# Optimization experiments

Measured on AMD Instinct MI355X. Metric: run time of the kernel, lower is better.

The kernel has to match this reference:

```python
import jax, jax.numpy as jnp
import numpy as np

D = 300       # word_embedding_dim
H = 15        # num_attention_heads
DK = D // H   # 20 per-head dim
QDIM = 200    # query_vector_dim (additive attention)
N_ITEMS = 100000
B, S = 1024, 50


def setup_inputs() -> dict:
    key = jax.random.key(0)
    ks = jax.random.split(key, 16)
    sc = 1.0 / np.sqrt(D)
    inp = {
        "user_news_id": jax.random.randint(ks[0], (B, S), 0, N_ITEMS, dtype=jnp.int64 if jax.config.jax_enable_x64 else jnp.int32),
        "user_vector": jax.random.normal(ks[1], (B, S, D), dtype=jnp.float32),
        # news-id embedding table, padding_idx=0 -> zero row
        "emb_table": jax.random.normal(ks[2], (N_ITEMS + 1, D), dtype=jnp.float32).at[0].set(0.0) * 0.02,
        # content Q/K/V projections
        "Wq": jax.random.normal(ks[3], (D, D), dtype=jnp.float32) * sc,
        "bq": jnp.zeros((D,), jnp.float32),
        "Wk": jax.random.normal(ks[4], (D, D), dtype=jnp.float32) * sc,
        "bk": jnp.zeros((D,), jnp.float32),
        "Wv": jax.random.normal(ks[5], (D, D), dtype=jnp.float32) * sc,
        "bv": jnp.zeros((D,), jnp.float32),
        # disentangled (news-id) Q/K projections
        "Wqp": jax.random.normal(ks[6], (D, D), dtype=jnp.float32) * sc,
        "bqp": jnp.zeros((D,), jnp.float32),
        "Wkp": jax.random.normal(ks[7], (D, D), dtype=jnp.float32) * sc,
        "bkp": jnp.zeros((D,), jnp.float32),
        # additive attention pooling params
        "W_add": jax.random.normal(ks[8], (D, QDIM), dtype=jnp.float32) * sc,
        "b_add": jnp.zeros((QDIM,), jnp.float32),
        "q_add": jax.random.normal(ks[9], (QDIM,), dtype=jnp.float32) * (1.0 / np.sqrt(QDIM)),
    }
    return inp


def _heads(x):
    # [B,S,D] -> [B,H,S,DK]
    b, s, _ = x.shape
    return x.reshape(b, s, H, DK).transpose(0, 2, 1, 3)


def reference(user_news_id, user_vector, emb_table, Wq, bq, Wk, bk, Wv, bv,
              Wqp, bqp, Wkp, bkp, W_add, b_add, q_add):
    # embedding lookup for clicked-news ids
    user_emb = emb_table[user_news_id]                      # [B,S,D]

    # content projections from user_vector, position/id projections from user_emb
    Qc = _heads(user_vector @ Wq + bq)
    Kc = _heads(user_vector @ Wk + bk)
    Vc = _heads(user_vector @ Wv + bv)
    Qp = _heads(user_emb @ Wqp + bqp)
    Kp = _heads(user_emb @ Wkp + bkp)

    # disentangled scores: content->content + content->id + id->content
    scores = (jnp.einsum("bhqd,bhkd->bhqk", Qc, Kc)
              + jnp.einsum("bhqd,bhkd->bhqk", Qc, Kp)
              + jnp.einsum("bhqd,bhkd->bhqk", Qp, Kc))
    scores = scores * (1.0 / np.sqrt(3.0 * DK))
    attn = jax.nn.softmax(scores, axis=-1)                  # [B,H,S,S]
    ctx = jnp.einsum("bhqk,bhkd->bhqd", attn, Vc)           # [B,H,S,DK]
    ctx = ctx.transpose(0, 2, 1, 3).reshape(user_vector.shape)  # [B,S,D]

    # additive attention pooling over the sequence
    t = jnp.tanh(ctx @ W_add + b_add)                       # [B,S,QDIM]
    a = jax.nn.softmax(t @ q_add, axis=-1)                  # [B,S]
    return jnp.einsum("bs,bsd->bd", a, ctx)                 # [B,D]
```

## Files before the change

kernel.cpp:

```cpp
#include <hip/hip_runtime.h>
#include <hip/hip_bf16.h>

#define SS   50
#define DD   300
#define NH   15
#define HD   20
#define QDIM 200

#define OFF_UV  0
#define OFF_UE  32800
#define QKSTR   400
#define OFF_Q   65600
#define OFF_K   85600
#define OFF_P   65600
#define PBLK    4608
#define PSTR    144
#define VTSTR   144
#define OFF_VT  105600
#define OFF_CTX 117120
#define OFF_LG  159104
#define OFF_A2  161152
#define OFF_IDS 161408
#define SM_TOTAL 161616

#define WSEG  97280
#define WAOFF 486400
#define WTOT  552960

typedef __attribute__((ext_vector_type(8)))  short bf8t;
typedef __attribute__((ext_vector_type(4)))  float f4t;
typedef __attribute__((ext_vector_type(16))) float f16t;

__device__ __forceinline__ unsigned short f2bf(float x){
  unsigned u = __float_as_uint(x);
  return (unsigned short)((u + 0x7fffu + ((u >> 16) & 1u)) >> 16);
}
__device__ __forceinline__ unsigned packbf(float a, float b){
  return (unsigned)f2bf(a) | ((unsigned)f2bf(b) << 16);
}
__device__ __forceinline__ f16t zero16(){
  f16t v;
  #pragma unroll
  for (int i = 0; i < 16; ++i) v[i] = 0.f;
  return v;
}

__global__ __launch_bounds__(256) void conv_weights(
    const float* __restrict__ Wq, const float* __restrict__ Wk,
    const float* __restrict__ Wv, const float* __restrict__ Wqp,
    const float* __restrict__ Wkp, const float* __restrict__ Wa,
    short* __restrict__ ws)
{
  int idx = blockIdx.x*256 + threadIdx.x;
  if (idx >= WTOT) return;
  float v = 0.f;
  if (idx < WAOFF){
    int seg = idx / WSEG, r = idx - seg*WSEG;
    int n = r / 320, k = r - n*320;
    const float* W = (seg==0)?Wq:(seg==1)?Wk:(seg==2)?Wv:(seg==3)?Wqp:Wkp;
    if (n < DD && k < DD) v = W[k*DD + n];
  } else {
    int r = idx - WAOFF;
    int n = r / 320, k = r - n*320;
    if (n < QDIM && k < DD) v = Wa[k*QDIM + n];
  }
  ws[idx] = (short)f2bf(v);
}

template<int NT, int NCTM>
__device__ __forceinline__ void gemm10(const unsigned char* sm, unsigned abase,
                                       const short* __restrict__ wt,
                                       int lane, int w, f4t (&acc)[NT][4])
{
  const int lm = lane & 15, lg = lane >> 4;
  #pragma unroll
  for (int step = 0; step < 10; ++step){
    bf8t a[4];
    #pragma unroll
    for (int rt = 0; rt < 4; ++rt)
      a[rt] = *(const bf8t*)(sm + abase + (unsigned)(rt*16 + lm)*656u + (unsigned)(step*32 + lg*8)*2u);
    #pragma unroll
    for (int t = 0; t < NT; ++t){
      int ct = w + t*8; if (ct > NCTM) ct = NCTM;
      bf8t bb = *(const bf8t*)(wt + (size_t)(ct*16 + lm)*320 + step*32 + lg*8);
      #pragma unroll
      for (int rt = 0; rt < 4; ++rt)
        acc[t][rt] = __builtin_amdgcn_mfma_f32_16x16x32_bf16(a[rt], bb, acc[t][rt], 0, 0, 0);
    }
  }
}

__global__ __launch_bounds__(512) void user_enc_kernel(
    const int*   __restrict__ ids, const float* __restrict__ uv,
    const float* __restrict__ emb,
    const float* __restrict__ bq, const float* __restrict__ bk,
    const float* __restrict__ bv, const float* __restrict__ bqp,
    const float* __restrict__ bkp,
    const float* __restrict__ ba, const float* __restrict__ qa,
    const short* __restrict__ wsb, float* __restrict__ out)
{
  __shared__ __align__(16) unsigned char sm[SM_TOTAL];
  const int tid  = threadIdx.x;
  const int b    = blockIdx.x;
  const int w    = tid >> 6;
  const int lane = tid & 63;
  const int lm   = lane & 15, lg = lane >> 4;
  const int l31  = lane & 31, hi = lane >> 5;

  const short* wqT  = wsb;
  const short* wkT  = wsb + WSEG;
  const short* wvT  = wsb + 2*WSEG;
  const short* wqpT = wsb + 3*WSEG;
  const short* wkpT = wsb + 4*WSEG;
  const short* waT  = wsb + WAOFF;

  if (tid < SS) *(int*)(sm + OFF_IDS + tid*4) = ids[(size_t)b*SS + tid];
  {
    const float* srcv = uv + (size_t)b*SS*DD;
    for (int i = tid; i < SS*75; i += 512){
      int s = i/75, j4 = i - s*75;
      float4 v = *(const float4*)(srcv + s*DD + j4*4);
      *(unsigned*)(sm + OFF_UV + (unsigned)s*656 + (unsigned)j4*8)     = packbf(v.x, v.y);
      *(unsigned*)(sm + OFF_UV + (unsigned)s*656 + (unsigned)j4*8 + 4) = packbf(v.z, v.w);
    }
    for (int i = tid; i < SS*28; i += 512){
      int s = i/28, j = i - s*28;
      unsigned off = (j < 14) ? (OFF_UV + (unsigned)s*656 + 600u + (unsigned)j*4)
                              : (OFF_UE + (unsigned)s*656 + 600u + (unsigned)(j-14)*4);
      *(unsigned*)(sm + off) = 0;
    }
    for (int i = tid; i < SS*14; i += 512)
      *(unsigned*)(sm + OFF_CTX + (unsigned)(i/14)*656 + 600u + (unsigned)(i%14)*4) = 0;
    for (int i = tid; i < 720; i += 512)
      *(float4*)(sm + OFF_VT + (unsigned)i*16) = make_float4(0.f,0.f,0.f,0.f);
  }
  __syncthreads();
  for (int i = tid; i < SS*75; i += 512){
    int s = i/75, j4 = i - s*75;
    int id = *(const int*)(sm + OFF_IDS + s*4);
    float4 v = *(const float4*)(emb + (size_t)id*DD + j4*4);
    *(unsigned*)(sm + OFF_UE + (unsigned)s*656 + (unsigned)j4*8)     = packbf(v.x, v.y);
    *(unsigned*)(sm + OFF_UE + (unsigned)s*656 + (unsigned)j4*8 + 4) = packbf(v.z, v.w);
  }

  const float rscale = 0.1290994449f;
  #pragma unroll 1
  for (int nb4 = 0; nb4 < 4; ++nb4){
    const int nheads = (nb4 < 3) ? 4 : 3;
    const int NCT    = (nb4 < 3) ? 5 : 4;
    __syncthreads();
    for (int i = tid; i < SS*4; i += 512){
      int r = i >> 2, hl0 = i & 3;
      *(float4*)(sm + OFF_Q + (unsigned)r*QKSTR + (unsigned)hl0*96 + 80) = make_float4(0.f,0.f,0.f,0.f);
      *(float4*)(sm + OFF_K + (unsigned)r*QKSTR + (unsigned)hl0*96 + 80) = make_float4(0.f,0.f,0.f,0.f);
    }
    for (int ht = w; ht < 8*NCT; ht += 8){
      const int g   = (ht >= 6*NCT) ? 3 : (ht >= 4*NCT) ? 2 : (ht >= 2*NCT) ? 1 : 0;
      const int rem = ht - g*2*NCT;
      const int c   = rem >> 1, rh = rem & 1;
      const int col = nb4*80 + c*16 + lm;
      const int colc = (col < DD) ? col : DD-1;
      const int head = col / HD;
      const int dd   = col - head*HD;
      const int hl   = head - nb4*4;
      const bool valid = (hl < nheads) && (col < DD);
      const unsigned abase = (g == 1) ? (unsigned)OFF_UE : (unsigned)OFF_UV;
      const short* wt = (g==0) ? wqT : (g==1) ? wqpT : (g==2) ? wvT : wkT;
      const short* wb = wt + (size_t)col*320 + lg*8;
      f4t a0 = {0.f,0.f,0.f,0.f}, a1 = {0.f,0.f,0.f,0.f};
      #pragma unroll
      for (int st = 0; st < 10; ++st){
        bf8t bb = *(const bf8t*)(wb + st*32);
        bf8t x0 = *(const bf8t*)(sm + abase + (unsigned)(rh*32 + lm)*656u + (unsigned)(st*32 + lg*8)*2u);
        bf8t x1 = *(const bf8t*)(sm + abase + (unsigned)(rh*32 + 16 + lm)*656u + (unsigned)(st*32 + lg*8)*2u);
        a0 = __builtin_amdgcn_mfma_f32_16x16x32_bf16(x0, bb, a0, 0, 0, 0);
        a1 = __builtin_amdgcn_mfma_f32_16x16x32_bf16(x1, bb, a1, 0, 0, 0);
      }
      if (g == 2){
        if (valid){
          float bias = bv[colc];
          unsigned vb = OFF_VT + (unsigned)(hl*HD + dd)*VTSTR;
          int r0 = rh*32 + lg*4;
          if (r0 < SS){
            *(unsigned*)(sm + vb + (unsigned)r0*2) = packbf(a0[0]+bias, a0[1]+bias);
            if (r0+2 < SS) *(unsigned*)(sm + vb + (unsigned)r0*2 + 4) = packbf(a0[2]+bias, a0[3]+bias);
          }
          int r1 = rh*32 + 16 + lg*4;
          if (r1 < SS){
            *(unsigned*)(sm + vb + (unsigned)r1*2) = packbf(a1[0]+bias, a1[1]+bias);
            if (r1+2 < SS) *(unsigned*)(sm + vb + (unsigned)r1*2 + 4) = packbf(a1[2]+bias, a1[3]+bias);
          }
        }
      } else if (g != 3){
        if (valid){
          float bias = (g==0) ? bq[colc] : bqp[colc];
          unsigned qb = OFF_Q + (unsigned)hl*96 + (unsigned)dd*2 + (g==1 ? 40u : 0u);
          #pragma unroll
          for (int i = 0; i < 4; ++i){
            int r0 = rh*32 + lg*4 + i;
            if (r0 < SS) *(unsigned short*)(sm + qb + (unsigned)r0*QKSTR) = f2bf(a0[i]+bias);
            int r1 = rh*32 + 16 + lg*4 + i;
            if (r1 < SS) *(unsigned short*)(sm + qb + (unsigned)r1*QKSTR) = f2bf(a1[i]+bias);
          }
        }
      } else {
        float bkc = bk[colc];
        if (valid){
          unsigned kb = OFF_K + (unsigned)hl*96 + (unsigned)dd*2 + 40u;
          #pragma unroll
          for (int i = 0; i < 4; ++i){
            int r0 = rh*32 + lg*4 + i;
            if (r0 < SS) *(unsigned short*)(sm + kb + (unsigned)r0*QKSTR) = f2bf(a0[i]+bkc);
            int r1 = rh*32 + 16 + lg*4 + i;
            if (r1 < SS) *(unsigned short*)(sm + kb + (unsigned)r1*QKSTR) = f2bf(a1[i]+bkc);
          }
        }
        const short* wb2 = wkpT + (size_t)col*320 + lg*8;
        #pragma unroll
        for (int st = 0; st < 10; ++st){
          bf8t bb = *(const bf8t*)(wb2 + st*32);
          bf8t x0 = *(const bf8t*)(sm + OFF_UE + (unsigned)(rh*32 + lm)*656u + (unsigned)(st*32 + lg*8)*2u);
          bf8t x1 = *(const bf8t*)(sm + OFF_UE + (unsigned)(rh*32 + 16 + lm)*656u + (unsigned)(st*32 + lg*8)*2u);
          a0 = __builtin_amdgcn_mfma_f32_16x16x32_bf16(x0, bb, a0, 0, 0, 0);
          a1 = __builtin_amdgcn_mfma_f32_16x16x32_bf16(x1, bb, a1, 0, 0, 0);
        }
        if (valid){
          float bsum = bkc + bkp[colc];
          unsigned kb = OFF_K + (unsigned)hl*96 + (unsigned)dd*2;
          #pragma unroll
          for (int i = 0; i < 4; ++i){
            int r0 = rh*32 + lg*4 + i;
            if (r0 < SS) *(unsigned short*)(sm + kb + (unsigned)r0*QKSTR) = f2bf(a0[i]+bsum);
            int r1 = rh*32 + 16 + lg*4 + i;
            if (r1 < SS) *(unsigned short*)(sm + kb + (unsigned)r1*QKSTR) = f2bf(a1[i]+bsum);
          }
        }
      }
    }
    __syncthreads();
    const int ahl = w >> 1, rt = w & 1;
    const bool act = (ahl < nheads);
    f16t s0, s1;
    if (act){
      s0 = zero16(); s1 = zero16();
      unsigned aoff = OFF_Q + (unsigned)(rt*32 + l31)*QKSTR + (unsigned)ahl*96 + (unsigned)hi*16;
      unsigned koff = OFF_K + (unsigned)l31*QKSTR + (unsigned)ahl*96 + (unsigned)hi*16;
      #pragma unroll
      for (int ks = 0; ks < 3; ++ks){
        bf8t a  = *(const bf8t*)(sm + aoff + ks*32);
        bf8t b0 = *(const bf8t*)(sm + koff + ks*32);
        bf8t b1 = *(const bf8t*)(sm + koff + 32u*QKSTR + ks*32);
        s0 = __builtin_amdgcn_mfma_f32_32x32x16_bf16(a, b0, s0, 0, 0, 0);
        s1 = __builtin_amdgcn_mfma_f32_32x32x16_bf16(a, b1, s1, 0, 0, 0);
      }
    }
    __syncthreads();
    if (act){
      const bool m1 = (l31 >= 18);
      unsigned pb = OFF_P + (unsigned)w*PBLK;
      float rinv[16];
      #pragma unroll
      for (int r = 0; r < 16; ++r){
        int lrow = (r&3) + 8*(r>>2) + 4*hi;
        float v0 = s0[r]*rscale;
        float v1 = m1 ? -INFINITY : s1[r]*rscale;
        float mx = fmaxf(v0, v1);
        #pragma unroll
        for (int off = 1; off <= 16; off <<= 1) mx = fmaxf(mx, __shfl_xor(mx, off));
        float e0 = __expf(v0 - mx);
        float e1 = m1 ? 0.f : __expf(v1 - mx);
        float sum = e0 + e1;
        #pragma unroll
        for (int off = 1; off <= 16; off <<= 1) sum += __shfl_xor(sum, off);
        rinv[r] = 1.0f/sum;
        *(unsigned short*)(sm + pb + (unsigned)lrow*PSTR + (unsigned)l31*2)      = f2bf(e0);
        *(unsigned short*)(sm + pb + (unsigned)lrow*PSTR + 64 + (unsigned)l31*2) = f2bf(e1);
      }
      f16t c = zero16();
      unsigned pa  = pb + (unsigned)l31*PSTR + (unsigned)hi*16;
      unsigned vb2 = OFF_VT + (unsigned)(ahl*HD + l31)*VTSTR + (unsigned)hi*16;
      #pragma unroll
      for (int ks = 0; ks < 4; ++ks){
        bf8t a = *(const bf8t*)(sm + pa + ks*32);
        bf8t v = *(const bf8t*)(sm + vb2 + ks*32);
        c = __builtin_amdgcn_mfma_f32_32x32x16_bf16(a, v, c, 0, 0, 0);
      }
      if (l31 < HD){
        int h = nb4*4 + ahl;
        #pragma unroll
        for (int r = 0; r < 16; ++r){
          int q = rt*32 + (r&3) + 8*(r>>2) + 4*hi;
          if (q < SS)
            *(unsigned short*)(sm + OFF_CTX + (unsigned)q*656 + (unsigned)(h*HD + l31)*2) =
                f2bf(c[r]*rinv[r]);
        }
      }
    }
  }
  __syncthreads();

  {
    f4t accp[2][4];
    #pragma unroll
    for (int t = 0; t < 2; ++t)
      #pragma unroll
      for (int r = 0; r < 4; ++r) accp[t][r] = (f4t){0.f,0.f,0.f,0.f};
    gemm10<2,12>(sm, OFF_CTX, waT, lane, w, accp);
    float part[4][4];
    #pragma unroll
    for (int rt2 = 0; rt2 < 4; ++rt2)
      #pragma unroll
      for (int i = 0; i < 4; ++i) part[rt2][i] = 0.f;
    #pragma unroll
    for (int t = 0; t < 2; ++t){
      int ct = w + t*8; if (ct > 12) ct = 12;
      bool valid = (t == 0) || (w < 5);
      int col = ct*16 + lm;
      float bav = (col < QDIM) ? ba[col] : 0.f;
      float qav = (valid && col < QDIM) ? qa[col] : 0.f;
      #pragma unroll
      for (int rt2 = 0; rt2 < 4; ++rt2)
        #pragma unroll
        for (int i = 0; i < 4; ++i)
          part[rt2][i] += tanhf(accp[t][rt2][i] + bav) * qav;
    }
    #pragma unroll
    for (int off = 1; off <= 8; off <<= 1)
      #pragma unroll
      for (int rt2 = 0; rt2 < 4; ++rt2)
        #pragma unroll
        for (int i = 0; i < 4; ++i)
          part[rt2][i] += __shfl_xor(part[rt2][i], off);
    if (lm == 0){
      #pragma unroll
      for (int rt2 = 0; rt2 < 4; ++rt2)
        #pragma unroll
        for (int i = 0; i < 4; ++i){
          int row = rt2*16 + lg*4 + i;
          if (row < SS) *(float*)(sm + OFF_LG + (unsigned)(row*8 + w)*4) = part[rt2][i];
        }
    }
  }
  __syncthreads();
  if (w == 0){
    const int sl = lane < SS ? lane : SS - 1;
    const bool rowok = lane < SS;
    float lgv = -INFINITY;
    if (rowok){
      float s = 0.f;
      #pragma unroll
      for (int j = 0; j < 8; ++j) s += *(const float*)(sm + OFF_LG + (unsigned)(sl*8 + j)*4);
      lgv = s;
    }
    float m = lgv;
    #pragma unroll
    for (int off = 32; off; off >>= 1) m = fmaxf(m, __shfl_xor(m, off));
    float e = rowok ? __expf(lgv - m) : 0.f;
    float ssum = e;
    #pragma unroll
    for (int off = 32; off; off >>= 1) ssum += __shfl_xor(ssum, off);
    *(float*)(sm + OFF_A2 + lane*4) = e / ssum;
  }
  __syncthreads();
  if (tid < DD){
    float accv = 0.f;
    for (int s = 0; s < SS; ++s){
      float av = *(const float*)(sm + OFF_A2 + (unsigned)s*4);
      unsigned short cv = *(const unsigned short*)(sm + OFF_CTX + (unsigned)s*656 + (unsigned)tid*2);
      accv = fmaf(av, __uint_as_float((unsigned)cv << 16), accv);
    }
    out[(size_t)b*DD + tid] = accv;
  }
}

extern "C" void kernel_launch(void* const* d_in, const int* in_sizes, int n_in,
                              void* d_out, int out_size, void* d_ws, size_t ws_size,
                              hipStream_t stream){
  (void)n_in; (void)ws_size; (void)out_size;
  const int*   ids = (const int*)  d_in[0];
  const float* uvp = (const float*)d_in[1];
  const float* emb = (const float*)d_in[2];
  const float* Wq  = (const float*)d_in[3];
  const float* bq  = (const float*)d_in[4];
  const float* Wk  = (const float*)d_in[5];
  const float* bk  = (const float*)d_in[6];
  const float* Wv  = (const float*)d_in[7];
  const float* bv  = (const float*)d_in[8];
  const float* Wqp = (const float*)d_in[9];
  const float* bqp = (const float*)d_in[10];
  const float* Wkp = (const float*)d_in[11];
  const float* bkp = (const float*)d_in[12];
  const float* Wa  = (const float*)d_in[13];
  const float* ba  = (const float*)d_in[14];
  const float* qa  = (const float*)d_in[15];
  short* wsb = (short*)d_ws;

  conv_weights<<<(WTOT + 255)/256, 256, 0, stream>>>(Wq, Wk, Wv, Wqp, Wkp, Wa, wsb);

  const int nblk = in_sizes[0] / SS;
  user_enc_kernel<<<nblk, 512, 0, stream>>>(ids, uvp, emb,
                                            bq, bk, bv, bqp, bkp, ba, qa,
                                            (const short*)wsb, (float*)d_out);
}
```

Baseline: 419.3 us.

## Split fused user encoder into projection, attention and pooling kernels

```diff
diff --git a/kernel.cpp b/kernel.cpp
--- a/kernel.cpp
+++ b/kernel.cpp
@@ -6,22 +6,6 @@
 #define NH   15
 #define HD   20
 #define QDIM 200
-
-#define OFF_UV  0
-#define OFF_UE  32800
-#define QKSTR   400
-#define OFF_Q   65600
-#define OFF_K   85600
-#define OFF_P   65600
-#define PBLK    4608
-#define PSTR    144
-#define VTSTR   144
-#define OFF_VT  105600
-#define OFF_CTX 117120
-#define OFF_LG  159104
-#define OFF_A2  161152
-#define OFF_IDS 161408
-#define SM_TOTAL 161616
 
 #define WSEG  97280
 #define WAOFF 486400
@@ -90,6 +74,363 @@
   }
 }
 
+#define K1_UV  0
+#define K1_UE  32800
+#define K1_IDS 74784
+#define K1_SM  74992
+
+__global__ __launch_bounds__(512) void k1_proj(
+    const int*   __restrict__ ids, const float* __restrict__ uv,
+    const float* __restrict__ emb,
+    const float* __restrict__ bq, const float* __restrict__ bk,
+    const float* __restrict__ bv, const float* __restrict__ bqp,
+    const float* __restrict__ bkp,
+    const short* __restrict__ wsb,
+    short* __restrict__ qg, short* __restrict__ kg, short* __restrict__ vg)
+{
+  __shared__ __align__(16) unsigned char sm[K1_SM];
+  const int tid  = threadIdx.x;
+  const int b    = blockIdx.x;
+  const int w    = tid >> 6;
+  const int lane = tid & 63;
+  const int lm   = lane & 15, lg = lane >> 4;
+
+  const short* wqT  = wsb;
+  const short* wkT  = wsb + WSEG;
+  const short* wvT  = wsb + 2*WSEG;
+  const short* wqpT = wsb + 3*WSEG;
+  const short* wkpT = wsb + 4*WSEG;
+
+  if (tid < SS) *(int*)(sm + K1_IDS + tid*4) = ids[(size_t)b*SS + tid];
+  {
+    const float* srcv = uv + (size_t)b*SS*DD;
+    for (int i = tid; i < SS*75; i += 512){
+      int s = i/75, j4 = i - s*75;
+      float4 v = *(const float4*)(srcv + s*DD + j4*4);
+      *(unsigned*)(sm + K1_UV + (unsigned)s*656 + (unsigned)j4*8)     = packbf(v.x, v.y);
+      *(unsigned*)(sm + K1_UV + (unsigned)s*656 + (unsigned)j4*8 + 4) = packbf(v.z, v.w);
+    }
+    for (int i = tid; i < SS*28; i += 512){
+      int s = i/28, j = i - s*28;
+      unsigned off = (j < 14) ? (K1_UV + (unsigned)s*656 + 600u + (unsigned)j*4)
+                              : (K1_UE + (unsigned)s*656 + 600u + (unsigned)(j-14)*4);
+      *(unsigned*)(sm + off) = 0;
+    }
+  }
+  __syncthreads();
+  for (int i = tid; i < SS*75; i += 512){
+    int s = i/75, j4 = i - s*75;
+    int id = *(const int*)(sm + K1_IDS + s*4);
+    float4 v = *(const float4*)(emb + (size_t)id*DD + j4*4);
+    *(unsigned*)(sm + K1_UE + (unsigned)s*656 + (unsigned)j4*8)     = packbf(v.x, v.y);
+    *(unsigned*)(sm + K1_UE + (unsigned)s*656 + (unsigned)j4*8 + 4) = packbf(v.z, v.w);
+  }
+  __syncthreads();
+
+  for (int i = tid; i < SS*15*4; i += 512){
+    int row = i / 60, r2 = i - row*60;
+    int head = r2 >> 2, j = r2 & 3;
+    size_t base = ((size_t)b*SS + row)*720 + head*48 + 40 + j*2;
+    *(unsigned*)(qg + base) = 0u;
+    *(unsigned*)(kg + base) = 0u;
+  }
+
+  for (int u = w; u < 152; u += 8){
+    const int g   = u / 38;
+    const int rem = u - g*38;
+    const int c   = rem >> 1, rh = rem & 1;
+    const int col  = c*16 + lm;
+    const int colc = (col < DD) ? col : DD-1;
+    const bool valid = (col < DD);
+    const int head = colc / HD;
+    const int dd   = colc - head*HD;
+    const unsigned abase = (g == 1) ? (unsigned)K1_UE : (unsigned)K1_UV;
+    const short* wt = (g==0) ? wqT : (g==1) ? wqpT : (g==2) ? wvT : wkT;
+    const short* wb = wt + (size_t)col*320 + lg*8;
+    f4t a0 = {0.f,0.f,0.f,0.f}, a1 = {0.f,0.f,0.f,0.f};
+    #pragma unroll
+    for (int st = 0; st < 10; ++st){
+      bf8t bb = *(const bf8t*)(wb + st*32);
+      bf8t x0 = *(const bf8t*)(sm + abase + (unsigned)(rh*32 + lm)*656u + (unsigned)(st*32 + lg*8)*2u);
+      bf8t x1 = *(const bf8t*)(sm + abase + (unsigned)(rh*32 + 16 + lm)*656u + (unsigned)(st*32 + lg*8)*2u);
+      a0 = __builtin_amdgcn_mfma_f32_16x16x32_bf16(x0, bb, a0, 0, 0, 0);
+      a1 = __builtin_amdgcn_mfma_f32_16x16x32_bf16(x1, bb, a1, 0, 0, 0);
+    }
+    if (g == 2){
+      if (valid){
+        float bias = bv[colc];
+        #pragma unroll
+        for (int i = 0; i < 4; ++i){
+          int r0 = rh*32 + lg*4 + i;
+          if (r0 < SS) vg[((size_t)b*SS + r0)*300 + col] = (short)f2bf(a0[i]+bias);
+          int r1 = rh*32 + 16 + lg*4 + i;
+          if (r1 < SS) vg[((size_t)b*SS + r1)*300 + col] = (short)f2bf(a1[i]+bias);
+        }
+      }
+    } else if (g != 3){
+      if (valid){
+        float bias = (g==0) ? bq[colc] : bqp[colc];
+        size_t qoff = (size_t)head*48 + dd + (g==1 ? 20 : 0);
+        #pragma unroll
+        for (int i = 0; i < 4; ++i){
+          int r0 = rh*32 + lg*4 + i;
+          if (r0 < SS) qg[((size_t)b*SS + r0)*720 + qoff] = (short)f2bf(a0[i]+bias);
+          int r1 = rh*32 + 16 + lg*4 + i;
+          if (r1 < SS) qg[((size_t)b*SS + r1)*720 + qoff] = (short)f2bf(a1[i]+bias);
+        }
+      }
+    } else {
+      float bkc = bk[colc];
+      if (valid){
+        size_t koff = (size_t)head*48 + 20 + dd;
+        #pragma unroll
+        for (int i = 0; i < 4; ++i){
+          int r0 = rh*32 + lg*4 + i;
+          if (r0 < SS) kg[((size_t)b*SS + r0)*720 + koff] = (short)f2bf(a0[i]+bkc);
+          int r1 = rh*32 + 16 + lg*4 + i;
+          if (r1 < SS) kg[((size_t)b*SS + r1)*720 + koff] = (short)f2bf(a1[i]+bkc);
+        }
+      }
+      const short* wb2 = wkpT + (size_t)col*320 + lg*8;
+      #pragma unroll
+      for (int st = 0; st < 10; ++st){
+        bf8t bb = *(const bf8t*)(wb2 + st*32);
+        bf8t x0 = *(const bf8t*)(sm + K1_UE + (unsigned)(rh*32 + lm)*656u + (unsigned)(st*32 + lg*8)*2u);
+        bf8t x1 = *(const bf8t*)(sm + K1_UE + (unsigned)(rh*32 + 16 + lm)*656u + (unsigned)(st*32 + lg*8)*2u);
+        a0 = __builtin_amdgcn_mfma_f32_16x16x32_bf16(x0, bb, a0, 0, 0, 0);
+        a1 = __builtin_amdgcn_mfma_f32_16x16x32_bf16(x1, bb, a1, 0, 0, 0);
+      }
+      if (valid){
+        float bsum = bkc + bkp[colc];
+        size_t koff = (size_t)head*48 + dd;
+        #pragma unroll
+        for (int i = 0; i < 4; ++i){
+          int r0 = rh*32 + lg*4 + i;
+          if (r0 < SS) kg[((size_t)b*SS + r0)*720 + koff] = (short)f2bf(a0[i]+bsum);
+          int r1 = rh*32 + 16 + lg*4 + i;
+          if (r1 < SS) kg[((size_t)b*SS + r1)*720 + koff] = (short)f2bf(a1[i]+bsum);
+        }
+      }
+    }
+  }
+}
+
+#define A_Q   0
+#define A_K   20000
+#define A_VT  40000
+#define A_PBLK 4608
+#define A_SM  53248
+
+__global__ __launch_bounds__(512) void k2_attn(
+    const short* __restrict__ qg, const short* __restrict__ kg,
+    const short* __restrict__ vg, short* __restrict__ cg)
+{
+  __shared__ __align__(16) unsigned char sm[A_SM];
+  const int tid  = threadIdx.x;
+  const int bid  = blockIdx.x;
+  const int b    = bid >> 2;
+  const int hg   = bid & 3;
+  const int nheads = (hg < 3) ? 4 : 3;
+  const int w    = tid >> 6;
+  const int lane = tid & 63;
+  const int l31  = lane & 31, hi = lane >> 5;
+
+  for (int i = tid; i < 828; i += 512)
+    *(float4*)(sm + A_VT + (unsigned)i*16) = make_float4(0.f,0.f,0.f,0.f);
+  __syncthreads();
+  for (int i = tid; i < 2400; i += 512){
+    int arr = (i < 1200) ? 0 : 1;
+    int j = i - arr*1200;
+    int row = j/24, c = j - row*24;
+    const short* src = (arr ? kg : qg) + ((size_t)b*SS + row)*720 + hg*192 + c*8;
+    float4 v = *(const float4*)src;
+    *(float4*)(sm + (arr ? A_K : A_Q) + (unsigned)row*400 + (unsigned)c*16) = v;
+  }
+  for (int i = tid; i < 2000; i += 512){
+    int row = i/40, d2 = i - row*40;
+    unsigned v = *(const unsigned*)(vg + ((size_t)b*SS + row)*300 + hg*80 + d2*2);
+    *(unsigned short*)(sm + A_VT + (unsigned)(d2*2)*144   + (unsigned)row*2) = (unsigned short)(v & 0xffffu);
+    *(unsigned short*)(sm + A_VT + (unsigned)(d2*2+1)*144 + (unsigned)row*2) = (unsigned short)(v >> 16);
+  }
+  __syncthreads();
+
+  const float rscale = 0.1290994449f;
+  const int ahl = w >> 1, rt = w & 1;
+  const bool act = (ahl < nheads);
+  f16t s0, s1;
+  if (act){
+    s0 = zero16(); s1 = zero16();
+    unsigned aoff = A_Q + (unsigned)(rt*32 + l31)*400 + (unsigned)ahl*96 + (unsigned)hi*16;
+    unsigned koff = A_K + (unsigned)l31*400 + (unsigned)ahl*96 + (unsigned)hi*16;
+    #pragma unroll
+    for (int ks = 0; ks < 3; ++ks){
+      bf8t a  = *(const bf8t*)(sm + aoff + ks*32);
+      bf8t b0 = *(const bf8t*)(sm + koff + ks*32);
+      bf8t b1 = *(const bf8t*)(sm + koff + 32u*400 + ks*32);
+      s0 = __builtin_amdgcn_mfma_f32_32x32x16_bf16(a, b0, s0, 0, 0, 0);
+      s1 = __builtin_amdgcn_mfma_f32_32x32x16_bf16(a, b1, s1, 0, 0, 0);
+    }
+  }
+  __syncthreads();
+  if (act){
+    const bool m1 = (l31 >= 18);
+    unsigned pb = (unsigned)w*A_PBLK;
+    float rinv[16];
+    #pragma unroll
+    for (int r = 0; r < 16; ++r){
+      int lrow = (r&3) + 8*(r>>2) + 4*hi;
+      float v0 = s0[r]*rscale;
+      float v1 = m1 ? -INFINITY : s1[r]*rscale;
+      float mx = fmaxf(v0, v1);
+      #pragma unroll
+      for (int off = 1; off <= 16; off <<= 1) mx = fmaxf(mx, __shfl_xor(mx, off));
+      float e0 = __expf(v0 - mx);
+      float e1 = m1 ? 0.f : __expf(v1 - mx);
+      float sum = e0 + e1;
+      #pragma unroll
+      for (int off = 1; off <= 16; off <<= 1) sum += __shfl_xor(sum, off);
+      rinv[r] = 1.0f/sum;
+      *(unsigned short*)(sm + pb + (unsigned)lrow*144 + (unsigned)l31*2)      = f2bf(e0);
+      *(unsigned short*)(sm + pb + (unsigned)lrow*144 + 64 + (unsigned)l31*2) = f2bf(e1);
+    }
+    f16t c = zero16();
+    unsigned pa  = pb + (unsigned)l31*144 + (unsigned)hi*16;
+    unsigned vb2 = A_VT + (unsigned)(ahl*HD + l31)*144 + (unsigned)hi*16;
+    #pragma unroll
+    for (int ks = 0; ks < 4; ++ks){
+      bf8t a = *(const bf8t*)(sm + pa + ks*32);
+      bf8t v = *(const bf8t*)(sm + vb2 + ks*32);
+      c = __builtin_amdgcn_mfma_f32_32x32x16_bf16(a, v, c, 0, 0, 0);
+    }
+    if (l31 < HD){
+      int h = hg*4 + ahl;
+      #pragma unroll
+      for (int r = 0; r < 16; ++r){
+        int q = rt*32 + (r&3) + 8*(r>>2) + 4*hi;
+        if (q < SS)
+          cg[((size_t)b*SS + q)*300 + h*HD + l31] = (short)f2bf(c[r]*rinv[r]);
+      }
+    }
+  }
+}
+
+#define B_CTX 0
+#define B_LG  41984
+#define B_A2  44032
+#define B_SM  44288
+
+__global__ __launch_bounds__(512) void k3_pool(
+    const short* __restrict__ cg, const short* __restrict__ wsb,
+    const float* __restrict__ ba, const float* __restrict__ qa,
+    float* __restrict__ out)
+{
+  __shared__ __align__(16) unsigned char sm[B_SM];
+  const int tid  = threadIdx.x;
+  const int b    = blockIdx.x;
+  const int w    = tid >> 6;
+  const int lane = tid & 63;
+  const int lm   = lane & 15, lg = lane >> 4;
+  const short* waT = wsb + WAOFF;
+
+  for (int i = tid; i < SS*75; i += 512){
+    int row = i/75, c = i - row*75;
+    uint2 v = *(const uint2*)(cg + ((size_t)b*SS + row)*300 + c*4);
+    *(uint2*)(sm + B_CTX + (unsigned)row*656 + (unsigned)c*8) = v;
+  }
+  for (int i = tid; i < SS*14; i += 512)
+    *(unsigned*)(sm + B_CTX + (unsigned)(i/14)*656 + 600u + (unsigned)(i%14)*4) = 0;
+  __syncthreads();
+
+  {
+    f4t accp[2][4];
+    #pragma unroll
+    for (int t = 0; t < 2; ++t)
+      #pragma unroll
+      for (int r = 0; r < 4; ++r) accp[t][r] = (f4t){0.f,0.f,0.f,0.f};
+    gemm10<2,12>(sm, B_CTX, waT, lane, w, accp);
+    float part[4][4];
+    #pragma unroll
+    for (int rt2 = 0; rt2 < 4; ++rt2)
+      #pragma unroll
+      for (int i = 0; i < 4; ++i) part[rt2][i] = 0.f;
+    #pragma unroll
+    for (int t = 0; t < 2; ++t){
+      int ct = w + t*8; if (ct > 12) ct = 12;
+      bool valid = (t == 0) || (w < 5);
+      int col = ct*16 + lm;
+      float bav = (col < QDIM) ? ba[col] : 0.f;
+      float qav = (valid && col < QDIM) ? qa[col] : 0.f;
+      #pragma unroll
+      for (int rt2 = 0; rt2 < 4; ++rt2)
+        #pragma unroll
+        for (int i = 0; i < 4; ++i)
+          part[rt2][i] += tanhf(accp[t][rt2][i] + bav) * qav;
+    }
+    #pragma unroll
+    for (int off = 1; off <= 8; off <<= 1)
+      #pragma unroll
+      for (int rt2 = 0; rt2 < 4; ++rt2)
+        #pragma unroll
+        for (int i = 0; i < 4; ++i)
+          part[rt2][i] += __shfl_xor(part[rt2][i], off);
+    if (lm == 0){
+      #pragma unroll
+      for (int rt2 = 0; rt2 < 4; ++rt2)
+        #pragma unroll
+        for (int i = 0; i < 4; ++i){
+          int row = rt2*16 + lg*4 + i;
+          if (row < SS) *(float*)(sm + B_LG + (unsigned)(row*8 + w)*4) = part[rt2][i];
+        }
+    }
+  }
+  __syncthreads();
+  if (w == 0){
+    const int sl = lane < SS ? lane : SS - 1;
+    const bool rowok = lane < SS;
+    float lgv = -INFINITY;
+    if (rowok){
+      float s = 0.f;
+      #pragma unroll
+      for (int j = 0; j < 8; ++j) s += *(const float*)(sm + B_LG + (unsigned)(sl*8 + j)*4);
+      lgv = s;
+    }
+    float m = lgv;
+    #pragma unroll
+    for (int off = 32; off; off >>= 1) m = fmaxf(m, __shfl_xor(m, off));
+    float e = rowok ? __expf(lgv - m) : 0.f;
+    float ssum = e;
+    #pragma unroll
+    for (int off = 32; off; off >>= 1) ssum += __shfl_xor(ssum, off);
+    *(float*)(sm + B_A2 + lane*4) = e / ssum;
+  }
+  __syncthreads();
+  if (tid < DD){
+    float accv = 0.f;
+    for (int s = 0; s < SS; ++s){
+      float av = *(const float*)(sm + B_A2 + (unsigned)s*4);
+      unsigned short cv = *(const unsigned short*)(sm + B_CTX + (unsigned)s*656 + (unsigned)tid*2);
+      accv = fmaf(av, __uint_as_float((unsigned)cv << 16), accv);
+    }
+    out[(size_t)b*DD + tid] = accv;
+  }
+}
+
+#define OFF_UV  0
+#define OFF_UE  32800
+#define QKSTR   400
+#define OFF_Q   65600
+#define OFF_K   85600
+#define OFF_P   65600
+#define PBLK    4608
+#define PSTR    144
+#define VTSTR   144
+#define OFF_VT  105600
+#define OFF_CTX 117120
+#define OFF_LG  159104
+#define OFF_A2  161152
+#define OFF_IDS 161408
+#define SM_TOTAL 161616
+
 __global__ __launch_bounds__(512) void user_enc_kernel(
     const int*   __restrict__ ids, const float* __restrict__ uv,
     const float* __restrict__ emb,
@@ -376,7 +717,7 @@
 extern "C" void kernel_launch(void* const* d_in, const int* in_sizes, int n_in,
                               void* d_out, int out_size, void* d_ws, size_t ws_size,
                               hipStream_t stream){
-  (void)n_in; (void)ws_size; (void)out_size;
+  (void)n_in; (void)out_size;
   const int*   ids = (const int*)  d_in[0];
   const float* uvp = (const float*)d_in[1];
   const float* emb = (const float*)d_in[2];
@@ -395,10 +736,28 @@
   const float* qa  = (const float*)d_in[15];
   short* wsb = (short*)d_ws;
 
+  const int nb = in_sizes[0] / SS;
+  const size_t wbytes = (size_t)WTOT * 2;
+  const size_t qelems = (size_t)nb * SS * 720;
+  const size_t velems = (size_t)nb * SS * 300;
+  const size_t need   = wbytes + 2*qelems*2 + 2*velems*2;
+
   conv_weights<<<(WTOT + 255)/256, 256, 0, stream>>>(Wq, Wk, Wv, Wqp, Wkp, Wa, wsb);
 
-  const int nblk = in_sizes[0] / SS;
-  user_enc_kernel<<<nblk, 512, 0, stream>>>(ids, uvp, emb,
+  if (ws_size >= need){
+    short* qg = (short*)((char*)d_ws + wbytes);
+    short* kg = qg + qelems;
+    short* vg = kg + qelems;
+    short* cg = vg + velems;
+    k1_proj<<<nb, 512, 0, stream>>>(ids, uvp, emb, bq, bk, bv, bqp, bkp,
+                                    (const short*)wsb, qg, kg, vg);
+    k2_attn<<<nb*4, 512, 0, stream>>>((const short*)qg, (const short*)kg,
+                                      (const short*)vg, cg);
+    k3_pool<<<nb, 512, 0, stream>>>((const short*)cg, (const short*)wsb,
+                                    ba, qa, (float*)d_out);
+  } else {
+    user_enc_kernel<<<nb, 512, 0, stream>>>(ids, uvp, emb,
                                             bq, bk, bv, bqp, bkp, ba, qa,
                                             (const short*)wsb, (float*)d_out);
-}
+  }
+}
```

Result: faster. 397.9 us (-5.1%).
